# Kernel optimization log

Measured on AMD Instinct MI355X. Metric: run time of the kernel, lower is better.

## Reference

```python
import jax, jax.numpy as jnp
import numpy as np

DIM = 16      # model width (hardcoded in source)
HEADS = 4
DH = DIM // HEADS  # 4, per-head dim
MLP = 4
L = 4         # encoder layers
OUT = 16      # mlp_head output
EPS = 1e-5


def _ln(x, g, b):
    mu = jnp.mean(x, axis=-1, keepdims=True)
    var = jnp.mean((x - mu) ** 2, axis=-1, keepdims=True)
    return (x - mu) * jax.lax.rsqrt(var + EPS) * g + b


def setup_inputs() -> dict:
    key = jax.random.key(0)
    ks = jax.random.split(key, 16)
    B, S = 256, 512
    s = 0.1
    return {
        "x": jax.random.normal(ks[0], (B, S, DIM), jnp.float32),
        "ln1_g": jnp.ones((L, DIM), jnp.float32),
        "ln1_b": jnp.zeros((L, DIM), jnp.float32),
        "in_w": jax.random.normal(ks[1], (L, 3 * DIM, DIM), jnp.float32) * s,
        "in_b": jax.random.normal(ks[2], (L, 3 * DIM), jnp.float32) * s,
        "out_w": jax.random.normal(ks[3], (L, DIM, DIM), jnp.float32) * s,
        "out_b": jax.random.normal(ks[4], (L, DIM), jnp.float32) * s,
        "ln2_g": jnp.ones((L, DIM), jnp.float32),
        "ln2_b": jnp.zeros((L, DIM), jnp.float32),
        "w1": jax.random.normal(ks[5], (L, MLP, DIM), jnp.float32) * s,
        "b1": jax.random.normal(ks[6], (L, MLP), jnp.float32) * s,
        "w2": jax.random.normal(ks[7], (L, DIM, MLP), jnp.float32) * s,
        "b2": jax.random.normal(ks[8], (L, DIM), jnp.float32) * s,
        "head_g": jnp.ones((DIM,), jnp.float32),
        "head_b": jnp.zeros((DIM,), jnp.float32),
        "head_w": jax.random.normal(ks[9], (OUT, DIM), jnp.float32) * s,
        "head_bias": jax.random.normal(ks[10], (OUT,), jnp.float32) * s,
    }


def reference(x, ln1_g, ln1_b, in_w, in_b, out_w, out_b,
              ln2_g, ln2_b, w1, b1, w2, b2,
              head_g, head_b, head_w, head_bias):
    B, S, _ = x.shape
    scale = 1.0 / np.sqrt(DH)
    for i in range(L):
        # --- pre-LN self-attention + residual (dropout=identity at inference)
        h = _ln(x, ln1_g[i], ln1_b[i])
        qkv = h @ in_w[i].T + in_b[i]                      # [B,S,3*DIM]
        q, k, v = jnp.split(qkv, 3, axis=-1)
        q = q.reshape(B, S, HEADS, DH).transpose(0, 2, 1, 3)  # [B,H,S,Dh]
        k = k.reshape(B, S, HEADS, DH).transpose(0, 2, 1, 3)
        v = v.reshape(B, S, HEADS, DH).transpose(0, 2, 1, 3)
        scores = jnp.einsum('bhsd,bhtd->bhst', q * scale, k)  # [B,H,S,S]
        attn = jax.nn.softmax(scores, axis=-1)
        o = jnp.einsum('bhst,bhtd->bhsd', attn, v)             # [B,H,S,Dh]
        o = o.transpose(0, 2, 1, 3).reshape(B, S, DIM)
        x = x + (o @ out_w[i].T + out_b[i])
        # --- pre-LN MLP + residual (exact GELU, as torch nn.GELU default)
        h = _ln(x, ln2_g[i], ln2_b[i])
        h = jax.nn.gelu(h @ w1[i].T + b1[i], approximate=False)
        x = x + (h @ w2[i].T + b2[i])
    cls = x[:, 0, :]                                          # [B,DIM]
    return _ln(cls, head_g, head_b) @ head_w.T + head_bias    # [B,OUT]
```

## Files before the change

kernel.cpp:

```cpp
#include <hip/hip_runtime.h>
#include <math.h>

#define NDIM 16
#define NMLP 4
#define NL 4
#define NOUT 16
#define NS 512
#define NT 1024
#define LEPS 1e-5f
#define VPAD 516

typedef __fp16 h2 __attribute__((ext_vector_type(2)));
typedef __fp16 h4 __attribute__((ext_vector_type(4)));
typedef float f32x4 __attribute__((ext_vector_type(4)));

__device__ __forceinline__ h2 pk2(float x, float y) {
    return __builtin_amdgcn_cvt_pkrtz(x, y);
}

__device__ __forceinline__ float fexp2(float x) {
#if __has_builtin(__builtin_amdgcn_exp2f)
    return __builtin_amdgcn_exp2f(x);
#else
    return exp2f(x);
#endif
}

#define MFMA16(a,b,c) __builtin_amdgcn_mfma_f32_16x16x16f16((a),(b),(c),0,0,0)

__global__ __launch_bounds__(NT)
void vit_fused(const float* __restrict__ gx,
               const float* __restrict__ g_ln1g, const float* __restrict__ g_ln1b,
               const float* __restrict__ g_inw,  const float* __restrict__ g_inb,
               const float* __restrict__ g_outw, const float* __restrict__ g_outb,
               const float* __restrict__ g_ln2g, const float* __restrict__ g_ln2b,
               const float* __restrict__ g_w1,   const float* __restrict__ g_b1,
               const float* __restrict__ g_w2,   const float* __restrict__ g_b2,
               const float* __restrict__ g_hg,   const float* __restrict__ g_hb,
               const float* __restrict__ g_hw,   const float* __restrict__ g_hbias,
               float* __restrict__ gout)
{
    __shared__ __align__(16) __fp16 sKh[NS][NDIM];
    __shared__ __align__(16) __fp16 sVT[NDIM][VPAD];
    __shared__ __align__(16) __fp16 sQO[NS][NDIM];
    __shared__ __align__(16) float sWiw[NL*48*NDIM];
    __shared__ float sWib[NL*48];
    __shared__ __align__(16) float sWow[NL*NDIM*NDIM];
    __shared__ float sWob[NL*NDIM];
    __shared__ float sLn1g[NL*NDIM], sLn1b[NL*NDIM], sLn2g[NL*NDIM], sLn2b[NL*NDIM];
    __shared__ __align__(16) float sW1[NL*NMLP*NDIM];
    __shared__ float sB1[NL*NMLP];
    __shared__ __align__(16) float sW2[NL*NDIM*NMLP];
    __shared__ float sB2[NL*NDIM];
    __shared__ float sHg[NDIM], sHb[NDIM];
    __shared__ __align__(16) float sHw[NOUT*NDIM];
    __shared__ float sHbias[NOUT];

    const int tid = threadIdx.x;
    const int t   = tid & (NS-1);
    const int hb  = (tid >> 9) << 3;
    const int b   = blockIdx.x;

    const int w  = tid >> 6;
    const int l  = tid & 63;
    const int g  = l >> 4;
    const int ql = l & 15;
    const int r0 = 32*w;

    for (int i = tid; i < NL*48*NDIM; i += NT) sWiw[i] = g_inw[i];
    for (int i = tid; i < NL*48;       i += NT) sWib[i] = g_inb[i];
    for (int i = tid; i < NL*NDIM*NDIM; i += NT) sWow[i] = g_outw[i];
    if (tid < NL*NDIM) {
        sWob[tid]  = g_outb[tid];
        sLn1g[tid] = g_ln1g[tid];  sLn1b[tid] = g_ln1b[tid];
        sLn2g[tid] = g_ln2g[tid];  sLn2b[tid] = g_ln2b[tid];
        sB2[tid]   = g_b2[tid];
    }
    for (int i = tid; i < NL*NMLP*NDIM; i += NT) { sW1[i] = g_w1[i]; sW2[i] = g_w2[i]; }
    if (tid < NL*NMLP) sB1[tid] = g_b1[tid];
    if (tid < NDIM)  { sHg[tid] = g_hg[tid]; sHb[tid] = g_hb[tid]; }
    if (tid < NOUT)    sHbias[tid] = g_hbias[tid];
    for (int i = tid; i < NOUT*NDIM; i += NT) sHw[i] = g_hw[i];

    float xr[NDIM];
    {
        const float4* xg4 = (const float4*)(gx + ((size_t)b*NS + t)*NDIM);
        float4 a = xg4[0], b4 = xg4[1], c4 = xg4[2], d4 = xg4[3];
        xr[0]=a.x;  xr[1]=a.y;  xr[2]=a.z;  xr[3]=a.w;
        xr[4]=b4.x; xr[5]=b4.y; xr[6]=b4.z; xr[7]=b4.w;
        xr[8]=c4.x; xr[9]=c4.y; xr[10]=c4.z; xr[11]=c4.w;
        xr[12]=d4.x; xr[13]=d4.y; xr[14]=d4.z; xr[15]=d4.w;
    }

    __syncthreads();

    for (int li = 0; li < NL; ++li) {
        float mu = 0.f;
        #pragma unroll
        for (int c = 0; c < NDIM; ++c) mu += xr[c];
        mu *= (1.f/NDIM);
        float var = 0.f;
        #pragma unroll
        for (int c = 0; c < NDIM; ++c) { float d = xr[c]-mu; var += d*d; }
        var *= (1.f/NDIM);
        float rs = rsqrtf(var + LEPS);
        float hn[NDIM];
        #pragma unroll
        for (int c = 0; c < NDIM; ++c)
            hn[c] = (xr[c]-mu)*rs*sLn1g[li*NDIM+c] + sLn1b[li*NDIM+c];

        const float* iw = &sWiw[li*48*NDIM];
        const float* ib = &sWib[li*48];

        {
            const float C = 0.72134752044448170368f;
            float qf[8];
            #pragma unroll
            for (int r = 0; r < 8; ++r) {
                const float* wrow = &iw[(hb+r)*NDIM];
                float acc = ib[hb+r];
                #pragma unroll
                for (int c = 0; c < NDIM; ++c) acc += hn[c]*wrow[c];
                qf[r] = acc*C;
            }
            h4 qlo = __builtin_shufflevector(pk2(qf[0],qf[1]), pk2(qf[2],qf[3]), 0,1,2,3);
            h4 qhi = __builtin_shufflevector(pk2(qf[4],qf[5]), pk2(qf[6],qf[7]), 0,1,2,3);
            *(h4*)&sQO[t][hb]   = qlo;
            *(h4*)&sQO[t][hb+4] = qhi;
        }
        {
            float kr[8];
            #pragma unroll
            for (int r = 0; r < 8; ++r) {
                const float* wrow = &iw[(16+hb+r)*NDIM];
                float acc = ib[16+hb+r];
                #pragma unroll
                for (int c = 0; c < NDIM; ++c) acc += hn[c]*wrow[c];
                kr[r] = acc;
            }
            h4 klo = __builtin_shufflevector(pk2(kr[0],kr[1]), pk2(kr[2],kr[3]), 0,1,2,3);
            h4 khi = __builtin_shufflevector(pk2(kr[4],kr[5]), pk2(kr[6],kr[7]), 0,1,2,3);
            *(h4*)&sKh[t][hb]   = klo;
            *(h4*)&sKh[t][hb+4] = khi;
        }
        {
            #pragma unroll
            for (int r = 0; r < 8; ++r) {
                const float* wrow = &iw[(32+hb+r)*NDIM];
                float acc = ib[32+hb+r];
                #pragma unroll
                for (int c = 0; c < NDIM; ++c) acc += hn[c]*wrow[c];
                sVT[hb+r][t] = (__fp16)acc;
            }
        }
        __syncthreads();

        {
            h4 z4 = {};
            h4 q4a = *(const h4*)&sQO[r0 + ql][4*g];
            h4 q4b = *(const h4*)&sQO[r0 + 16 + ql][4*g];
            h4 bqa[4], bqb[4];
            #pragma unroll
            for (int h = 0; h < 4; ++h) {
                bqa[h] = (g == h) ? q4a : z4;
                bqb[h] = (g == h) ? q4b : z4;
            }
            f32x4 zc = {0.f, 0.f, 0.f, 0.f};
            f32x4 acc[2][4];
            float sp[2][4];
            #pragma unroll
            for (int qt = 0; qt < 2; ++qt)
                #pragma unroll
                for (int h = 0; h < 4; ++h) { acc[qt][h] = zc; sp[qt][h] = 0.f; }

            for (int jt = 0; jt < NS/16; ++jt) {
                h4 ak = *(const h4*)&sKh[16*jt + ql][4*g];
                h4 av = *(const h4*)&sVT[ql][16*jt + 4*g];
                #pragma unroll
                for (int h = 0; h < 4; ++h) {
                    f32x4 T = MFMA16(ak, bqa[h], zc);
                    float p0 = fexp2(T[0]), p1 = fexp2(T[1]),
                          p2 = fexp2(T[2]), p3 = fexp2(T[3]);
                    sp[0][h] += (p0+p1)+(p2+p3);
                    h4 pb = __builtin_shufflevector(pk2(p0,p1), pk2(p2,p3), 0,1,2,3);
                    acc[0][h] = MFMA16(av, pb, acc[0][h]);

                    T = MFMA16(ak, bqb[h], zc);
                    p0 = fexp2(T[0]); p1 = fexp2(T[1]);
                    p2 = fexp2(T[2]); p3 = fexp2(T[3]);
                    sp[1][h] += (p0+p1)+(p2+p3);
                    pb = __builtin_shufflevector(pk2(p0,p1), pk2(p2,p3), 0,1,2,3);
                    acc[1][h] = MFMA16(av, pb, acc[1][h]);
                }
            }

            #pragma unroll
            for (int qt = 0; qt < 2; ++qt)
                #pragma unroll
                for (int h = 0; h < 4; ++h) {
                    float s = sp[qt][h];
                    s += __shfl_xor(s, 16);
                    s += __shfl_xor(s, 32);
                    sp[qt][h] = s;
                }

            #pragma unroll
            for (int qt = 0; qt < 2; ++qt) {
                float sg = (g < 2) ? ((g == 0) ? sp[qt][0] : sp[qt][1])
                                   : ((g == 2) ? sp[qt][2] : sp[qt][3]);
                f32x4 C = (g < 2) ? ((g == 0) ? acc[qt][0] : acc[qt][1])
                                  : ((g == 2) ? acc[qt][2] : acc[qt][3]);
                float inv = 1.f / sg;
                h4 o4 = __builtin_shufflevector(pk2(C[0]*inv, C[1]*inv),
                                                pk2(C[2]*inv, C[3]*inv), 0,1,2,3);
                *(h4*)&sQO[r0 + 16*qt + ql][4*g] = o4;
            }
        }
        __syncthreads();

        float of[NDIM];
        {
            float4 lo = *(const float4*)&sQO[t][0];
            float4 hi = *(const float4*)&sQO[t][8];
            const h2* l2  = (const h2*)&lo;
            const h2* h2p = (const h2*)&hi;
            #pragma unroll
            for (int i = 0; i < 4; ++i) {
                of[2*i]     = (float)l2[i].x;  of[2*i+1]   = (float)l2[i].y;
                of[8+2*i]   = (float)h2p[i].x; of[8+2*i+1] = (float)h2p[i].y;
            }
        }
        __syncthreads();

        {
            const float* ow = &sWow[li*NDIM*NDIM];
            const float* ob = &sWob[li*NDIM];
            #pragma unroll
            for (int c = 0; c < NDIM; ++c) {
                float acc = ob[c];
                #pragma unroll
                for (int k = 0; k < NDIM; ++k) acc += of[k]*ow[c*NDIM+k];
                xr[c] += acc;
            }
        }
        {
            float mu2 = 0.f;
            #pragma unroll
            for (int c = 0; c < NDIM; ++c) mu2 += xr[c];
            mu2 *= (1.f/NDIM);
            float var2 = 0.f;
            #pragma unroll
            for (int c = 0; c < NDIM; ++c) { float d = xr[c]-mu2; var2 += d*d; }
            var2 *= (1.f/NDIM);
            float rs2 = rsqrtf(var2 + LEPS);
            float hn2[NDIM];
            #pragma unroll
            for (int c = 0; c < NDIM; ++c)
                hn2[c] = (xr[c]-mu2)*rs2*sLn2g[li*NDIM+c] + sLn2b[li*NDIM+c];

            const float* w1p = &sW1[li*NMLP*NDIM];
            float h1[NMLP];
            #pragma unroll
            for (int m = 0; m < NMLP; ++m) {
                float acc = sB1[li*NMLP+m];
                #pragma unroll
                for (int c = 0; c < NDIM; ++c) acc += hn2[c]*w1p[m*NDIM+c];
                h1[m] = 0.5f*acc*(1.f + erff(acc*0.70710678118654752f));
            }
            const float* w2p = &sW2[li*NDIM*NMLP];
            #pragma unroll
            for (int c = 0; c < NDIM; ++c) {
                float acc = sB2[li*NDIM+c];
                #pragma unroll
                for (int m = 0; m < NMLP; ++m) acc += h1[m]*w2p[c*NMLP+m];
                xr[c] += acc;
            }
        }
    }

    if (tid == 0) {
        float mu = 0.f;
        #pragma unroll
        for (int c = 0; c < NDIM; ++c) mu += xr[c];
        mu *= (1.f/NDIM);
        float var = 0.f;
        #pragma unroll
        for (int c = 0; c < NDIM; ++c) { float d = xr[c]-mu; var += d*d; }
        var *= (1.f/NDIM);
        float rs = rsqrtf(var + LEPS);
        float hn[NDIM];
        #pragma unroll
        for (int c = 0; c < NDIM; ++c)
            hn[c] = (xr[c]-mu)*rs*sHg[c] + sHb[c];
        #pragma unroll
        for (int oi = 0; oi < NOUT; ++oi) {
            float acc = sHbias[oi];
            #pragma unroll
            for (int c = 0; c < NDIM; ++c) acc += hn[c]*sHw[oi*NDIM+c];
            gout[b*NOUT + oi] = acc;
        }
    }
}

extern "C" void kernel_launch(void* const* d_in, const int* in_sizes, int n_in,
                              void* d_out, int out_size, void* d_ws, size_t ws_size,
                              hipStream_t stream) {
    const float* x       = (const float*)d_in[0];
    const float* ln1_g   = (const float*)d_in[1];
    const float* ln1_b   = (const float*)d_in[2];
    const float* in_w    = (const float*)d_in[3];
    const float* in_b    = (const float*)d_in[4];
    const float* out_w   = (const float*)d_in[5];
    const float* out_b   = (const float*)d_in[6];
    const float* ln2_g   = (const float*)d_in[7];
    const float* ln2_b   = (const float*)d_in[8];
    const float* w1      = (const float*)d_in[9];
    const float* b1      = (const float*)d_in[10];
    const float* w2      = (const float*)d_in[11];
    const float* b2      = (const float*)d_in[12];
    const float* head_g  = (const float*)d_in[13];
    const float* head_b  = (const float*)d_in[14];
    const float* head_w  = (const float*)d_in[15];
    const float* head_bias = (const float*)d_in[16];
    float* out = (float*)d_out;

    const int B = in_sizes[0] / (NS * NDIM);

    vit_fused<<<B, NT, 0, stream>>>(x, ln1_g, ln1_b, in_w, in_b, out_w, out_b,
                                    ln2_g, ln2_b, w1, b1, w2, b2,
                                    head_g, head_b, head_w, head_bias, out);
}
```

Baseline: 183.4 us.

## Use 16x16x32 f16 MFMA for PV and dot2 for softmax row sums

Switches the attention inner loop from 16x16x16 MFMA to the gfx950 16x16x32 f16 MFMA. Each iteration now covers 32 keys, and the P·V product uses one K=32 MFMA instead of two K=16 ones. QK scores still need two MFMAs per 32 keys, with the operand zero-padded from 4 to 8 halves. The softmax denominators are accumulated with packed fp16 dot2 against ones, which rounds the probabilities to fp16 before summing. The launch bounds also gain a minimum of 4 blocks, which may force register caps or spills.

```diff
diff --git a/kernel.cpp b/kernel.cpp
--- a/kernel.cpp
+++ b/kernel.cpp
@@ -12,10 +12,19 @@
 
 typedef __fp16 h2 __attribute__((ext_vector_type(2)));
 typedef __fp16 h4 __attribute__((ext_vector_type(4)));
+typedef __fp16 h8 __attribute__((ext_vector_type(8)));
 typedef float f32x4 __attribute__((ext_vector_type(4)));
 
 __device__ __forceinline__ h2 pk2(float x, float y) {
     return __builtin_amdgcn_cvt_pkrtz(x, y);
+}
+
+__device__ __forceinline__ float fdot2(h2 a, h2 b, float c) {
+#if __has_builtin(__builtin_amdgcn_fdot2)
+    return __builtin_amdgcn_fdot2(a, b, c, false);
+#else
+    return (float)a.x * (float)b.x + (float)a.y * (float)b.y + c;
+#endif
 }
 
 __device__ __forceinline__ float fexp2(float x) {
@@ -26,9 +35,9 @@
 #endif
 }
 
-#define MFMA16(a,b,c) __builtin_amdgcn_mfma_f32_16x16x16f16((a),(b),(c),0,0,0)
-
-__global__ __launch_bounds__(NT)
+#define MFMA32(a,b,c) __builtin_amdgcn_mfma_f32_16x16x32_f16((a),(b),(c),0,0,0)
+
+__global__ __launch_bounds__(NT, 4)
 void vit_fused(const float* __restrict__ gx,
                const float* __restrict__ g_ln1g, const float* __restrict__ g_ln1b,
                const float* __restrict__ g_inw,  const float* __restrict__ g_inb,
@@ -157,13 +166,16 @@
 
         {
             h4 z4 = {};
+            h8 z8 = {};
             h4 q4a = *(const h4*)&sQO[r0 + ql][4*g];
             h4 q4b = *(const h4*)&sQO[r0 + 16 + ql][4*g];
-            h4 bqa[4], bqb[4];
+            h8 q8a = __builtin_shufflevector(q4a, z4, 0,1,2,3,4,5,6,7);
+            h8 q8b = __builtin_shufflevector(q4b, z4, 0,1,2,3,4,5,6,7);
+            h8 bqa[4], bqb[4];
             #pragma unroll
             for (int h = 0; h < 4; ++h) {
-                bqa[h] = (g == h) ? q4a : z4;
-                bqb[h] = (g == h) ? q4b : z4;
+                bqa[h] = (g == h) ? q8a : z8;
+                bqb[h] = (g == h) ? q8b : z8;
             }
             f32x4 zc = {0.f, 0.f, 0.f, 0.f};
             f32x4 acc[2][4];
@@ -172,25 +184,53 @@
             for (int qt = 0; qt < 2; ++qt)
                 #pragma unroll
                 for (int h = 0; h < 4; ++h) { acc[qt][h] = zc; sp[qt][h] = 0.f; }
-
-            for (int jt = 0; jt < NS/16; ++jt) {
-                h4 ak = *(const h4*)&sKh[16*jt + ql][4*g];
-                h4 av = *(const h4*)&sVT[ql][16*jt + 4*g];
+            h2 one2; one2.x = (__fp16)1.0f; one2.y = (__fp16)1.0f;
+
+            for (int jj = 0; jj < NS; jj += 32) {
+                h4 ak0 = *(const h4*)&sKh[jj + ql][4*g];
+                h4 ak1 = *(const h4*)&sKh[jj + 16 + ql][4*g];
+                h8 a0 = __builtin_shufflevector(ak0, z4, 0,1,2,3,4,5,6,7);
+                h8 a1 = __builtin_shufflevector(ak1, z4, 0,1,2,3,4,5,6,7);
+                h4 av0 = *(const h4*)&sVT[ql][jj + 4*g];
+                h4 av1 = *(const h4*)&sVT[ql][jj + 16 + 4*g];
+                h8 av  = __builtin_shufflevector(av0, av1, 0,1,2,3,4,5,6,7);
+
                 #pragma unroll
                 for (int h = 0; h < 4; ++h) {
-                    f32x4 T = MFMA16(ak, bqa[h], zc);
-                    float p0 = fexp2(T[0]), p1 = fexp2(T[1]),
-                          p2 = fexp2(T[2]), p3 = fexp2(T[3]);
-                    sp[0][h] += (p0+p1)+(p2+p3);
-                    h4 pb = __builtin_shufflevector(pk2(p0,p1), pk2(p2,p3), 0,1,2,3);
-                    acc[0][h] = MFMA16(av, pb, acc[0][h]);
-
-                    T = MFMA16(ak, bqb[h], zc);
-                    p0 = fexp2(T[0]); p1 = fexp2(T[1]);
-                    p2 = fexp2(T[2]); p3 = fexp2(T[3]);
-                    sp[1][h] += (p0+p1)+(p2+p3);
-                    pb = __builtin_shufflevector(pk2(p0,p1), pk2(p2,p3), 0,1,2,3);
-                    acc[1][h] = MFMA16(av, pb, acc[1][h]);
+                    {
+                        f32x4 T0 = MFMA32(a0, bqa[h], zc);
+                        f32x4 T1 = MFMA32(a1, bqa[h], zc);
+                        h2 p0 = pk2(fexp2(T0[0]), fexp2(T0[1]));
+                        h2 p1 = pk2(fexp2(T0[2]), fexp2(T0[3]));
+                        h2 p2 = pk2(fexp2(T1[0]), fexp2(T1[1]));
+                        h2 p3 = pk2(fexp2(T1[2]), fexp2(T1[3]));
+                        sp[0][h] = fdot2(p0, one2,
+                                   fdot2(p1, one2,
+                                   fdot2(p2, one2,
+                                   fdot2(p3, one2, sp[0][h]))));
+                        h8 pb = __builtin_shufflevector(
+                                    __builtin_shufflevector(p0, p1, 0,1,2,3),
+                                    __builtin_shufflevector(p2, p3, 0,1,2,3),
+                                    0,1,2,3,4,5,6,7);
+                        acc[0][h] = MFMA32(av, pb, acc[0][h]);
+                    }
+                    {
+                        f32x4 T0 = MFMA32(a0, bqb[h], zc);
+                        f32x4 T1 = MFMA32(a1, bqb[h], zc);
+                        h2 p0 = pk2(fexp2(T0[0]), fexp2(T0[1]));
+                        h2 p1 = pk2(fexp2(T0[2]), fexp2(T0[3]));
+                        h2 p2 = pk2(fexp2(T1[0]), fexp2(T1[1]));
+                        h2 p3 = pk2(fexp2(T1[2]), fexp2(T1[3]));
+                        sp[1][h] = fdot2(p0, one2,
+                                   fdot2(p1, one2,
+                                   fdot2(p2, one2,
+                                   fdot2(p3, one2, sp[1][h]))));
+                        h8 pb = __builtin_shufflevector(
+                                    __builtin_shufflevector(p0, p1, 0,1,2,3),
+                                    __builtin_shufflevector(p2, p3, 0,1,2,3),
+                                    0,1,2,3,4,5,6,7);
+                        acc[1][h] = MFMA32(av, pb, acc[1][h]);
+                    }
                 }
             }
 
```

Result: faster. 179.2 us (-2.3%).
